# Kernel tuning notes

Measured on AMD Instinct MI355X. Metric: run time of the kernel, lower is better.

## Reference

```python
import jax, jax.numpy as jnp
import numpy as np


def setup_inputs() -> dict:
    key = jax.random.key(0)
    k1, k2, k3 = jax.random.split(key, 3)
    B, S, D = 8, 1024, 128
    logits = jax.random.normal(k1, (B, S, D), dtype=jnp.float32)
    labels = jax.random.normal(k2, (B, S, D), dtype=jnp.float32)
    # all-valid mask: any fully-padded row would make the softmax row all -inf (NaN),
    # matching the original torch behavior; ones keeps the baseline finite.
    pad_mask = jnp.ones((B, S), dtype=jnp.int32)
    ad_idxs = jax.random.randint(k3, (B, S), 0, 1000, dtype=jnp.int64)
    return {"logits": logits, "labels": labels, "pad_mask": pad_mask, "ad_idxs": ad_idxs}


def reference(logits, labels, pad_mask, ad_idxs):
    B, S, D = logits.shape
    N = B * S
    logits_flat = logits.reshape(N, D)
    labels_flat = labels.reshape(N, D)
    valid = pad_mask.reshape(N).astype(bool)
    ad = ad_idxs.reshape(N)

    # [N, N] pairwise similarity
    sim = logits_flat @ labels_flat.T
    pair_valid = valid[:, None] & valid[None, :]
    sim = jnp.where(pair_valid, sim, -jnp.inf)

    sim_prob = jax.nn.softmax(sim, axis=-1)

    label_mat = ((ad[:, None] == ad[None, :]) & pair_valid).astype(sim_prob.dtype)
    EPS = 1e-12
    pos_loss = -jnp.log2(jnp.clip(sim_prob, EPS)) * label_mat
    loss = pos_loss.sum(axis=-1).mean()
    return loss
```

## Files before the change

kernel.cpp:

```cpp
#include <hip/hip_runtime.h>
#include <math.h>

#define N 8192
#define D 128
#define NCHUNK 32
#define CHUNK_COLS (N / NCHUNK)
#define NBUCKET 1000
#define MAXB 48

#define CLIP_TERM 39.86313713864835f
#define LOG2E     1.4426950408889634f

typedef short bf16x8 __attribute__((ext_vector_type(8)));
typedef float f32x4  __attribute__((ext_vector_type(4)));

static __device__ __forceinline__ unsigned short f2bf(float f) {
    unsigned u = __builtin_bit_cast(unsigned, f);
    u += 0x7FFFu + ((u >> 16) & 1u);
    return (unsigned short)(u >> 16);
}

static __device__ __forceinline__ float exp2_fast(float x) {
    return __builtin_amdgcn_exp2f(x);
}

__global__ void convert_kernel(const float* __restrict__ a,
                               const float* __restrict__ b,
                               uint4* __restrict__ A,
                               uint4* __restrict__ B,
                               float* __restrict__ l_total,
                               float* __restrict__ out) {
    const int t = blockIdx.x * 256 + threadIdx.x;
    if (t < N) l_total[t] = 0.0f;
    if (t == 0) *out = 0.0f;
    const int half = N * D / 8;
    const bool first = t < half;
    const int u = first ? t : t - half;
    const int r = u >> 4, k8 = u & 15;
    const float4* src = first ? (const float4*)a : (const float4*)b;
    float4 v0 = src[u * 2], v1 = src[u * 2 + 1];
    if (first) {
        v0.x *= LOG2E; v0.y *= LOG2E; v0.z *= LOG2E; v0.w *= LOG2E;
        v1.x *= LOG2E; v1.y *= LOG2E; v1.z *= LOG2E; v1.w *= LOG2E;
    }
    union { unsigned short us[8]; uint4 v; } p;
    p.us[0] = f2bf(v0.x); p.us[1] = f2bf(v0.y); p.us[2] = f2bf(v0.z); p.us[3] = f2bf(v0.w);
    p.us[4] = f2bf(v1.x); p.us[5] = f2bf(v1.y); p.us[6] = f2bf(v1.z); p.us[7] = f2bf(v1.w);
    const int chunk = ((r >> 4) * 4 + (k8 >> 2)) * 64 + (k8 & 3) * 16 + (r & 15);
    (first ? A : B)[chunk] = p.v;
}

__global__ __launch_bounds__(256, 2)
void sim_lse_kernel(const uint4* __restrict__ Ach,
                    const uint4* __restrict__ Bch,
                    float* __restrict__ l_total) {
    const int tid = threadIdx.x;
    const int lane = tid & 63;
    const int w = tid >> 6;
    const int quad = lane >> 4;
    const int rowBase = blockIdx.x * 256 + w * 64;
    const int col0 = blockIdx.y * CHUNK_COLS;
    const int rtile0 = rowBase >> 4;

    bf16x8 afr[4][4];
#pragma unroll
    for (int rt = 0; rt < 4; ++rt)
#pragma unroll
        for (int kt = 0; kt < 4; ++kt)
            afr[rt][kt] = __builtin_bit_cast(bf16x8,
                Ach[((rtile0 + rt) * 4 + kt) * 64 + lane]);

    float l[16];
#pragma unroll
    for (int s = 0; s < 16; ++s) l[s] = 0.0f;

#pragma unroll 2
    for (int cs = 0; cs < CHUNK_COLS / 32; ++cs) {
        const int ctile0 = (col0 >> 4) + cs * 2;

        bf16x8 bfr[2][4];
#pragma unroll
        for (int ct = 0; ct < 2; ++ct)
#pragma unroll
            for (int kt = 0; kt < 4; ++kt)
                bfr[ct][kt] = __builtin_bit_cast(bf16x8,
                    Bch[((ctile0 + ct) * 4 + kt) * 64 + lane]);

        f32x4 acc[4][2];
#pragma unroll
        for (int rt = 0; rt < 4; ++rt) { acc[rt][0] = (f32x4)(0.0f); acc[rt][1] = (f32x4)(0.0f); }

#pragma unroll
        for (int kt = 0; kt < 4; ++kt)
#pragma unroll
            for (int rt = 0; rt < 4; ++rt) {
                acc[rt][0] = __builtin_amdgcn_mfma_f32_16x16x32_bf16(afr[rt][kt], bfr[0][kt], acc[rt][0], 0, 0, 0);
                acc[rt][1] = __builtin_amdgcn_mfma_f32_16x16x32_bf16(afr[rt][kt], bfr[1][kt], acc[rt][1], 0, 0, 0);
            }

#pragma unroll
        for (int rt = 0; rt < 4; ++rt)
#pragma unroll
            for (int reg = 0; reg < 4; ++reg)
                l[rt * 4 + reg] += exp2_fast(acc[rt][0][reg]) + exp2_fast(acc[rt][1][reg]);
    }

#pragma unroll
    for (int s = 0; s < 16; ++s) {
        float ls = l[s];
#pragma unroll
        for (int off = 1; off < 16; off <<= 1) ls += __shfl_xor(ls, off, 64);
        if ((lane & 15) == 0) {
            const int rg = rowBase + (s >> 2) * 16 + quad * 4 + (s & 3);
            atomicAdd(&l_total[rg], ls);
        }
    }
}

__global__ __launch_bounds__(256)
void pos_finalize_kernel(const float* __restrict__ logits,
                         const float* __restrict__ labels,
                         const int* __restrict__ ad,
                         const float* __restrict__ l_total,
                         float* __restrict__ out) {
    __shared__ float4 Lg[MAXB * 32];
    __shared__ float4 Lb[MAXB * 32];
    __shared__ int rows[MAXB];
    __shared__ float lseS[MAXB];
    __shared__ int nb_sh;
    __shared__ float red[4];
    const int tid = threadIdx.x;
    const int bId = blockIdx.x;

    if (tid == 0) nb_sh = 0;
    __syncthreads();
#pragma unroll
    for (int it = 0; it < N / 256; ++it) {
        const int r = it * 256 + tid;
        if (ad[r] == bId) {
            const int slot = atomicAdd(&nb_sh, 1);
            if (slot < MAXB) rows[slot] = r;
        }
    }
    __syncthreads();
    const int nb = min(nb_sh, MAXB);
    if (nb == 0) return;

    for (int idx = tid; idx < nb * 32; idx += 256) {
        const int rl = idx >> 5, c = idx & 31;
        const int rg = rows[rl];
        Lg[rl * 32 + c] = ((const float4*)logits)[rg * 32 + c];
        Lb[rl * 32 + c] = ((const float4*)labels)[rg * 32 + c];
        if (c == 0) lseS[rl] = log2f(l_total[rg]);
    }
    __syncthreads();

    float sum = 0.0f;
    const int pairs = nb * nb;
    for (int p = tid; p < pairs; p += 256) {
        const int i = p / nb, j = p - i * nb;
        float sx = 0.f, sy = 0.f, sz = 0.f, sw = 0.f;
#pragma unroll 8
        for (int c = 0; c < 32; ++c) {
            const float4 x = Lg[i * 32 + c];
            const float4 y = Lb[j * 32 + c];
            sx = fmaf(x.x, y.x, sx); sy = fmaf(x.y, y.y, sy);
            sz = fmaf(x.z, y.z, sz); sw = fmaf(x.w, y.w, sw);
        }
        const float simlog2 = ((sx + sy) + (sz + sw)) * LOG2E;
        sum += fminf(lseS[i] - simlog2, CLIP_TERM);
    }

#pragma unroll
    for (int off = 32; off >= 1; off >>= 1) sum += __shfl_xor(sum, off, 64);
    const int lane = tid & 63, wid = tid >> 6;
    if (lane == 0) red[wid] = sum;
    __syncthreads();
    if (tid == 0)
        atomicAdd(out, (red[0] + red[1] + red[2] + red[3]) * (1.0f / (float)N));
}

extern "C" void kernel_launch(void* const* d_in, const int* in_sizes, int n_in,
                              void* d_out, int out_size, void* d_ws, size_t ws_size,
                              hipStream_t stream) {
    const float* logits = (const float*)d_in[0];
    const float* labels = (const float*)d_in[1];
    const int* ad = (const int*)d_in[3];
    float* out = (float*)d_out;

    uint4* Ach = (uint4*)d_ws;
    uint4* Bch = Ach + N * D / 8;
    float* l_total = (float*)(Bch + N * D / 8);

    convert_kernel<<<2 * N * D / 8 / 256, 256, 0, stream>>>(
        logits, labels, Ach, Bch, l_total, out);
    dim3 g(N / 256, NCHUNK);
    sim_lse_kernel<<<g, 256, 0, stream>>>(Ach, Bch, l_total);
    pos_finalize_kernel<<<NBUCKET, 256, 0, stream>>>(logits, labels, ad, l_total, out);
}
```

Before: 117.5 us.

## Fuse logits bf16 conversion into sim kernel and halve column chunk count

The logits fp32→bf16 conversion, including the log2e scaling, moves out of the pre-pass and into the sim_lse kernel's A-fragment load, so the convert kernel now handles only the labels. The grid's column dimension drops from 32 to 16 chunks, with each block covering 512 columns. This removes the workspace write and re-read for A and halves how often A fragments and the row atomics are redone. The cost is uncoalesced strided fp32 loads of A, done per block, and fewer blocks in flight.

```diff
diff --git a/kernel.cpp b/kernel.cpp
--- a/kernel.cpp
+++ b/kernel.cpp
@@ -3,8 +3,6 @@
 
 #define N 8192
 #define D 128
-#define NCHUNK 32
-#define CHUNK_COLS (N / NCHUNK)
 #define NBUCKET 1000
 #define MAXB 48
 
@@ -24,58 +22,58 @@
     return __builtin_amdgcn_exp2f(x);
 }
 
-__global__ void convert_kernel(const float* __restrict__ a,
-                               const float* __restrict__ b,
-                               uint4* __restrict__ A,
-                               uint4* __restrict__ B,
+__global__ void convert_kernel(const float* __restrict__ b,
+                               uint4* __restrict__ Bch,
                                float* __restrict__ l_total,
                                float* __restrict__ out) {
     const int t = blockIdx.x * 256 + threadIdx.x;
     if (t < N) l_total[t] = 0.0f;
     if (t == 0) *out = 0.0f;
-    const int half = N * D / 8;
-    const bool first = t < half;
-    const int u = first ? t : t - half;
-    const int r = u >> 4, k8 = u & 15;
-    const float4* src = first ? (const float4*)a : (const float4*)b;
-    float4 v0 = src[u * 2], v1 = src[u * 2 + 1];
-    if (first) {
-        v0.x *= LOG2E; v0.y *= LOG2E; v0.z *= LOG2E; v0.w *= LOG2E;
-        v1.x *= LOG2E; v1.y *= LOG2E; v1.z *= LOG2E; v1.w *= LOG2E;
-    }
+    const int r = t >> 4, k8 = t & 15;
+    const float4 v0 = ((const float4*)b)[t * 2];
+    const float4 v1 = ((const float4*)b)[t * 2 + 1];
     union { unsigned short us[8]; uint4 v; } p;
     p.us[0] = f2bf(v0.x); p.us[1] = f2bf(v0.y); p.us[2] = f2bf(v0.z); p.us[3] = f2bf(v0.w);
     p.us[4] = f2bf(v1.x); p.us[5] = f2bf(v1.y); p.us[6] = f2bf(v1.z); p.us[7] = f2bf(v1.w);
     const int chunk = ((r >> 4) * 4 + (k8 >> 2)) * 64 + (k8 & 3) * 16 + (r & 15);
-    (first ? A : B)[chunk] = p.v;
+    Bch[chunk] = p.v;
 }
 
 __global__ __launch_bounds__(256, 2)
-void sim_lse_kernel(const uint4* __restrict__ Ach,
+void sim_lse_kernel(const float* __restrict__ logits,
                     const uint4* __restrict__ Bch,
                     float* __restrict__ l_total) {
     const int tid = threadIdx.x;
     const int lane = tid & 63;
     const int w = tid >> 6;
     const int quad = lane >> 4;
+    const int l16 = lane & 15;
     const int rowBase = blockIdx.x * 256 + w * 64;
-    const int col0 = blockIdx.y * CHUNK_COLS;
-    const int rtile0 = rowBase >> 4;
+    const int col0 = blockIdx.y * 512;
 
     bf16x8 afr[4][4];
 #pragma unroll
-    for (int rt = 0; rt < 4; ++rt)
+    for (int rt = 0; rt < 4; ++rt) {
+        const float* rp = logits + (size_t)(rowBase + rt * 16 + l16) * D;
 #pragma unroll
-        for (int kt = 0; kt < 4; ++kt)
-            afr[rt][kt] = __builtin_bit_cast(bf16x8,
-                Ach[((rtile0 + rt) * 4 + kt) * 64 + lane]);
+        for (int kt = 0; kt < 4; ++kt) {
+            const float4 a0 = *(const float4*)(rp + kt * 32 + quad * 8);
+            const float4 a1 = *(const float4*)(rp + kt * 32 + quad * 8 + 4);
+            union { unsigned short us[8]; bf16x8 v; } u;
+            u.us[0] = f2bf(a0.x * LOG2E); u.us[1] = f2bf(a0.y * LOG2E);
+            u.us[2] = f2bf(a0.z * LOG2E); u.us[3] = f2bf(a0.w * LOG2E);
+            u.us[4] = f2bf(a1.x * LOG2E); u.us[5] = f2bf(a1.y * LOG2E);
+            u.us[6] = f2bf(a1.z * LOG2E); u.us[7] = f2bf(a1.w * LOG2E);
+            afr[rt][kt] = u.v;
+        }
+    }
 
     float l[16];
 #pragma unroll
     for (int s = 0; s < 16; ++s) l[s] = 0.0f;
 
 #pragma unroll 2
-    for (int cs = 0; cs < CHUNK_COLS / 32; ++cs) {
+    for (int cs = 0; cs < 16; ++cs) {
         const int ctile0 = (col0 >> 4) + cs * 2;
 
         bf16x8 bfr[2][4];
@@ -110,7 +108,7 @@
         float ls = l[s];
 #pragma unroll
         for (int off = 1; off < 16; off <<= 1) ls += __shfl_xor(ls, off, 64);
-        if ((lane & 15) == 0) {
+        if (l16 == 0) {
             const int rg = rowBase + (s >> 2) * 16 + quad * 4 + (s & 3);
             atomicAdd(&l_total[rg], ls);
         }
@@ -188,13 +186,11 @@
     const int* ad = (const int*)d_in[3];
     float* out = (float*)d_out;
 
-    uint4* Ach = (uint4*)d_ws;
-    uint4* Bch = Ach + N * D / 8;
+    uint4* Bch = (uint4*)d_ws;
     float* l_total = (float*)(Bch + N * D / 8);
 
-    convert_kernel<<<2 * N * D / 8 / 256, 256, 0, stream>>>(
-        logits, labels, Ach, Bch, l_total, out);
-    dim3 g(N / 256, NCHUNK);
-    sim_lse_kernel<<<g, 256, 0, stream>>>(Ach, Bch, l_total);
+    convert_kernel<<<N * D / 8 / 256, 256, 0, stream>>>(labels, Bch, l_total, out);
+    dim3 g(N / 256, 16);
+    sim_lse_kernel<<<g, 256, 0, stream>>>(logits, Bch, l_total);
     pos_finalize_kernel<<<NBUCKET, 256, 0, stream>>>(logits, labels, ad, l_total, out);
 }
```

New measurement: 122.3 us. 4.0% more time.

## Precompute ad-index bucket lists and remap sim blocks for XCD-local column chunks

Applied to the files above, without the earlier changes.

Bucket membership lists are now built during the conversion kernel with global atomics, which the finalize kernel reads directly. Before, each of the 1000 finalize blocks scanned all 8192 ad indices. The sim kernel also switches to a 1D grid whose block-id mapping places column chunks so blocks on the same XCD share B-chunk data in L2. This adds a memset launch and global atomic contention in the convert kernel. Row order within a bucket becomes nondeterministic, but the loss is order-invariant.

```diff
diff --git a/kernel.cpp b/kernel.cpp
--- a/kernel.cpp
+++ b/kernel.cpp
@@ -28,10 +28,18 @@
                                const float* __restrict__ b,
                                uint4* __restrict__ A,
                                uint4* __restrict__ B,
+                               const int* __restrict__ ad,
+                               int* __restrict__ bcnt,
+                               int* __restrict__ blist,
                                float* __restrict__ l_total,
                                float* __restrict__ out) {
     const int t = blockIdx.x * 256 + threadIdx.x;
-    if (t < N) l_total[t] = 0.0f;
+    if (t < N) {
+        l_total[t] = 0.0f;
+        const int bv = ad[t];
+        const int slot = atomicAdd(&bcnt[bv], 1);
+        if (slot < MAXB) blist[bv * MAXB + slot] = t;
+    }
     if (t == 0) *out = 0.0f;
     const int half = N * D / 8;
     const bool first = t < half;
@@ -58,8 +66,13 @@
     const int lane = tid & 63;
     const int w = tid >> 6;
     const int quad = lane >> 4;
-    const int rowBase = blockIdx.x * 256 + w * 64;
-    const int col0 = blockIdx.y * CHUNK_COLS;
+    const int bid = blockIdx.x;
+    const int xcd = bid & 7;
+    const int slot = bid >> 3;
+    const int colChunk = xcd + 8 * (slot & 3);
+    const int rowBlock = slot >> 2;
+    const int rowBase = rowBlock * 256 + w * 64;
+    const int col0 = colChunk * CHUNK_COLS;
     const int rtile0 = rowBase >> 4;
 
     bf16x8 afr[4][4];
@@ -120,31 +133,21 @@
 __global__ __launch_bounds__(256)
 void pos_finalize_kernel(const float* __restrict__ logits,
                          const float* __restrict__ labels,
-                         const int* __restrict__ ad,
+                         const int* __restrict__ bcnt,
+                         const int* __restrict__ blist,
                          const float* __restrict__ l_total,
                          float* __restrict__ out) {
     __shared__ float4 Lg[MAXB * 32];
     __shared__ float4 Lb[MAXB * 32];
     __shared__ int rows[MAXB];
     __shared__ float lseS[MAXB];
-    __shared__ int nb_sh;
     __shared__ float red[4];
     const int tid = threadIdx.x;
     const int bId = blockIdx.x;
-
-    if (tid == 0) nb_sh = 0;
+    const int nb = min(bcnt[bId], MAXB);
+    if (nb == 0) return;
+    if (tid < nb) rows[tid] = blist[bId * MAXB + tid];
     __syncthreads();
-#pragma unroll
-    for (int it = 0; it < N / 256; ++it) {
-        const int r = it * 256 + tid;
-        if (ad[r] == bId) {
-            const int slot = atomicAdd(&nb_sh, 1);
-            if (slot < MAXB) rows[slot] = r;
-        }
-    }
-    __syncthreads();
-    const int nb = min(nb_sh, MAXB);
-    if (nb == 0) return;
 
     for (int idx = tid; idx < nb * 32; idx += 256) {
         const int rl = idx >> 5, c = idx & 31;
@@ -191,10 +194,13 @@
     uint4* Ach = (uint4*)d_ws;
     uint4* Bch = Ach + N * D / 8;
     float* l_total = (float*)(Bch + N * D / 8);
-
+    int* bcnt = (int*)(l_total + N);
+    int* blist = bcnt + NBUCKET;
+
+    hipMemsetAsync(bcnt, 0, NBUCKET * sizeof(int), stream);
     convert_kernel<<<2 * N * D / 8 / 256, 256, 0, stream>>>(
-        logits, labels, Ach, Bch, l_total, out);
-    dim3 g(N / 256, NCHUNK);
-    sim_lse_kernel<<<g, 256, 0, stream>>>(Ach, Bch, l_total);
-    pos_finalize_kernel<<<NBUCKET, 256, 0, stream>>>(logits, labels, ad, l_total, out);
-}
+        logits, labels, Ach, Bch, ad, bcnt, blist, l_total, out);
+    sim_lse_kernel<<<1024, 256, 0, stream>>>(Ach, Bch, l_total);
+    pos_finalize_kernel<<<NBUCKET, 256, 0, stream>>>(logits, labels, bcnt, blist,
+                                                     l_total, out);
+}
```

Result: faster. 113.8 us (-3.1%).
